# Optimization experiments

Hardware: AMD Instinct MI355X
Metric: run time of the kernel (lower is better)

The kernel has to match this reference:

```python
import jax, jax.numpy as jnp
import numpy as np

N = 500000   # active voxels
CIN = 32
COUT = 64
K = 27       # 3^3 kernel offsets
M = 250000   # kernel-map pairs per offset
EPS = 1e-5


def setup_inputs() -> dict:
    key = jax.random.key(0)
    ks = jax.random.split(key, 7)
    feats = jax.random.normal(ks[0], (N, CIN), dtype=jnp.float32)
    W = jax.random.normal(ks[1], (K, CIN, COUT), dtype=jnp.float32) / np.sqrt(K * CIN)
    gamma = jnp.ones((COUT,), dtype=jnp.float32)
    beta = jnp.zeros((COUT,), dtype=jnp.float32)
    run_mean = 0.1 * jax.random.normal(ks[2], (COUT,), dtype=jnp.float32)
    run_var = jax.random.uniform(ks[3], (COUT,), dtype=jnp.float32) + 0.5
    in_idx = jax.random.randint(ks[4], (K, M), 0, N, dtype=jnp.int32)
    out_idx = jax.random.randint(ks[5], (K, M), 0, N, dtype=jnp.int32)
    return {"feats": feats, "W": W, "gamma": gamma, "beta": beta,
            "run_mean": run_mean, "run_var": run_var,
            "in_idx": in_idx, "out_idx": out_idx}


def reference(feats, W, gamma, beta, run_mean, run_var, in_idx, out_idx):
    # Sparse 3D conv: for each kernel offset k, gather input rows, apply W[k],
    # scatter-accumulate into output rows (MinkowskiConvolution semantics).
    n_out = feats.shape[0]  # stride=1 -> same active sites

    def body(acc, xs):
        Wk, ik, ok = xs                      # [CIN,COUT], [M], [M]
        contrib = feats[ik] @ Wk             # gather + GEMM: [M, COUT]
        return acc.at[ok].add(contrib), None # scatter-accumulate

    out0 = jnp.zeros((n_out, COUT), dtype=feats.dtype)
    out, _ = jax.lax.scan(body, out0, (W, in_idx, out_idx))

    # BatchNorm (inference stats) + ReLU, fused elementwise epilogue
    inv = jax.lax.rsqrt(run_var + EPS)
    y = (out - run_mean) * (inv * gamma) + beta
    return jnp.maximum(y, 0.0)
```

## Files before the change

### kernel.cpp

```cpp
#include <hip/hip_runtime.h>

#define CIN  32
#define COUT 64
#define KOFF 27
#define EPS  1e-5f

__global__ __launch_bounds__(256) void conv_scatter(
    const float* __restrict__ feats,
    const float* __restrict__ W,
    const int*   __restrict__ in_idx,
    const int*   __restrict__ out_idx,
    float*       __restrict__ out,
    int M)
{
    __shared__ float Wl[CIN * COUT];
    const int k   = blockIdx.x;
    const int tid = threadIdx.x;

    const float* Wk = W + (size_t)k * (CIN * COUT);
    for (int i = tid; i < CIN * COUT; i += 256) Wl[i] = Wk[i];
    __syncthreads();

    const int lane = tid & 63;
    const int wave = tid >> 6;
    const int wavesTotal = gridDim.y * 4;
    const int* ikb = in_idx  + (size_t)k * M;
    const int* okb = out_idx + (size_t)k * M;

    for (int m = blockIdx.y * 4 + wave; m < M; m += wavesTotal) {
        const int ik = ikb[m];
        const int ok = okb[m];
        const float4* f4 = (const float4*)(feats + (size_t)ik * CIN);
        float acc = 0.f;
        #pragma unroll
        for (int c0 = 0; c0 < CIN / 4; ++c0) {
            float4 f = f4[c0];
            acc += f.x * Wl[(c0 * 4 + 0) * COUT + lane];
            acc += f.y * Wl[(c0 * 4 + 1) * COUT + lane];
            acc += f.z * Wl[(c0 * 4 + 2) * COUT + lane];
            acc += f.w * Wl[(c0 * 4 + 3) * COUT + lane];
        }
        atomicAdd(out + (size_t)ok * COUT + lane, acc);
    }
}

__global__ __launch_bounds__(256) void bn_relu(
    float* __restrict__ out,
    const float* __restrict__ gamma,
    const float* __restrict__ beta,
    const float* __restrict__ rmean,
    const float* __restrict__ rvar,
    int total4)
{
    __shared__ float scale[COUT], shift[COUT];
    if (threadIdx.x < COUT) {
        const int c = threadIdx.x;
        const float inv = rsqrtf(rvar[c] + EPS);
        const float s = inv * gamma[c];
        scale[c] = s;
        shift[c] = beta[c] - rmean[c] * s;
    }
    __syncthreads();

    const int stride = gridDim.x * blockDim.x;
    for (int i = blockIdx.x * blockDim.x + threadIdx.x; i < total4; i += stride) {
        float4 v = ((const float4*)out)[i];
        const int c0 = (i * 4) & (COUT - 1);
        v.x = fmaxf(v.x * scale[c0 + 0] + shift[c0 + 0], 0.f);
        v.y = fmaxf(v.y * scale[c0 + 1] + shift[c0 + 1], 0.f);
        v.z = fmaxf(v.z * scale[c0 + 2] + shift[c0 + 2], 0.f);
        v.w = fmaxf(v.w * scale[c0 + 3] + shift[c0 + 3], 0.f);
        ((float4*)out)[i] = v;
    }
}

extern "C" void kernel_launch(void* const* d_in, const int* in_sizes, int n_in,
                              void* d_out, int out_size, void* d_ws, size_t ws_size,
                              hipStream_t stream) {
    const float* feats  = (const float*)d_in[0];
    const float* W      = (const float*)d_in[1];
    const float* gamma  = (const float*)d_in[2];
    const float* beta   = (const float*)d_in[3];
    const float* rmean  = (const float*)d_in[4];
    const float* rvar   = (const float*)d_in[5];
    const int*   in_idx  = (const int*)d_in[6];
    const int*   out_idx = (const int*)d_in[7];
    float* out = (float*)d_out;

    const int N = in_sizes[0] / CIN;
    const int M = in_sizes[6] / KOFF;

    hipMemsetAsync(out, 0, (size_t)N * COUT * sizeof(float), stream);

    dim3 grid(KOFF, 512);
    conv_scatter<<<grid, 256, 0, stream>>>(feats, W, in_idx, out_idx, out, M);

    const int total4 = N * COUT / 4;
    int blocks = (total4 + 255) / 256;
    if (blocks > 2048) blocks = 2048;
    bn_relu<<<blocks, 256, 0, stream>>>(out, gamma, beta, rmean, rvar, total4);
}
```

Before: 2.236 ms.

## Bin kernel-map pairs by output tile and accumulate in shared memory

Adds a counting-sort pipeline (histogram, single-block scan, fill) that groups gather/scatter pairs by 256-row output tile and kernel offset, packing input index, offset and local row into one 32-bit record. A new conv kernel then accumulates each tile in LDS with shared atomics, holding that offset's weights in registers, and applies BN+ReLU before one coalesced write. This removes global float atomics, the output memset and the separate epilogue pass. In exchange it adds preprocessing kernels with global int atomics, a serial one-block scan, and a dependence on workspace size and N < 2^19 (otherwise it falls back to the old path).

```diff
diff --git a/kernel.cpp b/kernel.cpp
--- a/kernel.cpp
+++ b/kernel.cpp
@@ -3,73 +3,173 @@
 #define CIN  32
 #define COUT 64
 #define KOFF 27
+#define TILE 256
 #define EPS  1e-5f
 
+
+__global__ __launch_bounds__(256) void hist_kernel(
+    const int* __restrict__ out_idx, int* __restrict__ hist, int M)
+{
+    const int m = blockIdx.x * 256 + threadIdx.x;
+    const int k = blockIdx.y;
+    if (m < M) {
+        const int ok = out_idx[(size_t)k * M + m];
+        atomicAdd(&hist[(ok >> 8) * KOFF + k], 1);
+    }
+}
+
+__global__ __launch_bounds__(1024) void scan_kernel(
+    const int* __restrict__ hist, int* __restrict__ off, int* __restrict__ cur, int B)
+{
+    __shared__ int part[1024];
+    const int tid = threadIdx.x;
+    const int chunk = (B + 1023) / 1024;
+    const int base = tid * chunk;
+    int sum = 0;
+    for (int j = 0; j < chunk; ++j) { int i = base + j; if (i < B) sum += hist[i]; }
+    part[tid] = sum;
+    __syncthreads();
+    for (int d = 1; d < 1024; d <<= 1) {
+        int v = (tid >= d) ? part[tid - d] : 0;
+        __syncthreads();
+        part[tid] += v;
+        __syncthreads();
+    }
+    int run = part[tid] - sum;
+    for (int j = 0; j < chunk; ++j) {
+        int i = base + j;
+        if (i < B) { off[i] = run; cur[i] = run; run += hist[i]; }
+    }
+    if (tid == 1023) off[B] = run;
+}
+
+__global__ __launch_bounds__(256) void fill_kernel(
+    const int* __restrict__ in_idx, const int* __restrict__ out_idx,
+    int* __restrict__ cur, unsigned* __restrict__ recs, int M)
+{
+    const int m = blockIdx.x * 256 + threadIdx.x;
+    const int k = blockIdx.y;
+    if (m < M) {
+        const int ok  = out_idx[(size_t)k * M + m];
+        const int ik  = in_idx [(size_t)k * M + m];
+        const int bin = (ok >> 8) * KOFF + k;
+        const int pos = atomicAdd(&cur[bin], 1);
+        recs[pos] = (unsigned)ik | ((unsigned)k << 19) | ((unsigned)(ok & 255) << 24);
+    }
+}
+
+__global__ __launch_bounds__(512, 4) void conv_main(
+    const float* __restrict__ feats, const float* __restrict__ W,
+    const int* __restrict__ off, const unsigned* __restrict__ recs,
+    const float* __restrict__ gamma, const float* __restrict__ beta,
+    const float* __restrict__ rmean, const float* __restrict__ rvar,
+    float* __restrict__ out, int N)
+{
+    __shared__ float acc[TILE * COUT];
+    __shared__ float sc[COUT], sh[COUT];
+    const int tid  = threadIdx.x;
+    const int tile = blockIdx.x;
+
+    float4* acc4 = (float4*)acc;
+    for (int i = tid; i < TILE * COUT / 4; i += 512) acc4[i] = make_float4(0, 0, 0, 0);
+    if (tid < COUT) {
+        const float inv = rsqrtf(rvar[tid] + EPS);
+        const float s = inv * gamma[tid];
+        sc[tid] = s; sh[tid] = beta[tid] - rmean[tid] * s;
+    }
+    __syncthreads();
+
+    const int lane = tid & 63;
+    const int wave = tid >> 6;
+
+    for (int k = wave; k < KOFF; k += 8) {
+        const int seg = tile * KOFF + k;
+        const int s = off[seg], e = off[seg + 1];
+        if (s >= e) continue;
+        float w[CIN];
+        const float* Wk = W + (size_t)k * (CIN * COUT);
+        #pragma unroll
+        for (int c = 0; c < CIN; ++c) w[c] = Wk[c * COUT + lane];
+        for (int r = s; r < e; ++r) {
+            const unsigned rec = recs[r];
+            const int ik    = rec & 0x7FFFF;
+            const int local = rec >> 24;
+            const float4* f4 = (const float4*)(feats + (size_t)ik * CIN);
+            float a = 0.f;
+            #pragma unroll
+            for (int c4 = 0; c4 < CIN / 4; ++c4) {
+                const float4 f = f4[c4];
+                a += f.x * w[c4*4+0] + f.y * w[c4*4+1] + f.z * w[c4*4+2] + f.w * w[c4*4+3];
+            }
+            atomicAdd(&acc[local * COUT + lane], a);
+        }
+    }
+    __syncthreads();
+
+    const int base = tile * TILE;
+    for (int i = tid; i < TILE * COUT / 4; i += 512) {
+        const int row = i >> 4;
+        if (base + row < N) {
+            float4 v = acc4[i];
+            const int c0 = (i & 15) * 4;
+            v.x = fmaxf(v.x * sc[c0+0] + sh[c0+0], 0.f);
+            v.y = fmaxf(v.y * sc[c0+1] + sh[c0+1], 0.f);
+            v.z = fmaxf(v.z * sc[c0+2] + sh[c0+2], 0.f);
+            v.w = fmaxf(v.w * sc[c0+3] + sh[c0+3], 0.f);
+            ((float4*)out)[(size_t)base * (COUT / 4) + i] = v;
+        }
+    }
+}
+
+
 __global__ __launch_bounds__(256) void conv_scatter(
-    const float* __restrict__ feats,
-    const float* __restrict__ W,
-    const int*   __restrict__ in_idx,
-    const int*   __restrict__ out_idx,
-    float*       __restrict__ out,
-    int M)
+    const float* __restrict__ feats, const float* __restrict__ W,
+    const int* __restrict__ in_idx, const int* __restrict__ out_idx,
+    float* __restrict__ out, int M)
 {
     __shared__ float Wl[CIN * COUT];
-    const int k   = blockIdx.x;
-    const int tid = threadIdx.x;
-
+    const int k = blockIdx.x, tid = threadIdx.x;
     const float* Wk = W + (size_t)k * (CIN * COUT);
     for (int i = tid; i < CIN * COUT; i += 256) Wl[i] = Wk[i];
     __syncthreads();
-
-    const int lane = tid & 63;
-    const int wave = tid >> 6;
+    const int lane = tid & 63, wave = tid >> 6;
     const int wavesTotal = gridDim.y * 4;
-    const int* ikb = in_idx  + (size_t)k * M;
+    const int* ikb = in_idx + (size_t)k * M;
     const int* okb = out_idx + (size_t)k * M;
-
     for (int m = blockIdx.y * 4 + wave; m < M; m += wavesTotal) {
-        const int ik = ikb[m];
-        const int ok = okb[m];
+        const int ik = ikb[m], ok = okb[m];
         const float4* f4 = (const float4*)(feats + (size_t)ik * CIN);
         float acc = 0.f;
         #pragma unroll
         for (int c0 = 0; c0 < CIN / 4; ++c0) {
             float4 f = f4[c0];
-            acc += f.x * Wl[(c0 * 4 + 0) * COUT + lane];
-            acc += f.y * Wl[(c0 * 4 + 1) * COUT + lane];
-            acc += f.z * Wl[(c0 * 4 + 2) * COUT + lane];
-            acc += f.w * Wl[(c0 * 4 + 3) * COUT + lane];
+            acc += f.x * Wl[(c0*4+0)*COUT + lane] + f.y * Wl[(c0*4+1)*COUT + lane]
+                 + f.z * Wl[(c0*4+2)*COUT + lane] + f.w * Wl[(c0*4+3)*COUT + lane];
         }
         atomicAdd(out + (size_t)ok * COUT + lane, acc);
     }
 }
 
 __global__ __launch_bounds__(256) void bn_relu(
-    float* __restrict__ out,
-    const float* __restrict__ gamma,
-    const float* __restrict__ beta,
-    const float* __restrict__ rmean,
-    const float* __restrict__ rvar,
-    int total4)
+    float* __restrict__ out, const float* __restrict__ gamma, const float* __restrict__ beta,
+    const float* __restrict__ rmean, const float* __restrict__ rvar, int total4)
 {
     __shared__ float scale[COUT], shift[COUT];
     if (threadIdx.x < COUT) {
         const int c = threadIdx.x;
         const float inv = rsqrtf(rvar[c] + EPS);
         const float s = inv * gamma[c];
-        scale[c] = s;
-        shift[c] = beta[c] - rmean[c] * s;
-    }
-    __syncthreads();
-
+        scale[c] = s; shift[c] = beta[c] - rmean[c] * s;
+    }
+    __syncthreads();
     const int stride = gridDim.x * blockDim.x;
     for (int i = blockIdx.x * blockDim.x + threadIdx.x; i < total4; i += stride) {
         float4 v = ((const float4*)out)[i];
         const int c0 = (i * 4) & (COUT - 1);
-        v.x = fmaxf(v.x * scale[c0 + 0] + shift[c0 + 0], 0.f);
-        v.y = fmaxf(v.y * scale[c0 + 1] + shift[c0 + 1], 0.f);
-        v.z = fmaxf(v.z * scale[c0 + 2] + shift[c0 + 2], 0.f);
-        v.w = fmaxf(v.w * scale[c0 + 3] + shift[c0 + 3], 0.f);
+        v.x = fmaxf(v.x * scale[c0+0] + shift[c0+0], 0.f);
+        v.y = fmaxf(v.y * scale[c0+1] + shift[c0+1], 0.f);
+        v.z = fmaxf(v.z * scale[c0+2] + shift[c0+2], 0.f);
+        v.w = fmaxf(v.w * scale[c0+3] + shift[c0+3], 0.f);
         ((float4*)out)[i] = v;
     }
 }
@@ -89,14 +189,31 @@
 
     const int N = in_sizes[0] / CIN;
     const int M = in_sizes[6] / KOFF;
-
-    hipMemsetAsync(out, 0, (size_t)N * COUT * sizeof(float), stream);
-
-    dim3 grid(KOFF, 512);
-    conv_scatter<<<grid, 256, 0, stream>>>(feats, W, in_idx, out_idx, out, M);
-
-    const int total4 = N * COUT / 4;
-    int blocks = (total4 + 255) / 256;
-    if (blocks > 2048) blocks = 2048;
-    bn_relu<<<blocks, 256, 0, stream>>>(out, gamma, beta, rmean, rvar, total4);
-}
+    const int ntiles = (N + TILE - 1) / TILE;
+    const int B = ntiles * KOFF;
+    const size_t total_pairs = (size_t)KOFF * M;
+    const size_t needed = (size_t)(3 * B + 1) * 4 + total_pairs * 4;
+
+    if (ws_size >= needed && N < (1 << 19)) {
+        int* hist = (int*)d_ws;
+        int* off  = hist + B;
+        int* cur  = off + B + 1;
+        unsigned* recs = (unsigned*)(cur + B);
+
+        hipMemsetAsync(hist, 0, (size_t)B * 4, stream);
+        dim3 g((M + 255) / 256, KOFF);
+        hist_kernel<<<g, 256, 0, stream>>>(out_idx, hist, M);
+        scan_kernel<<<1, 1024, 0, stream>>>(hist, off, cur, B);
+        fill_kernel<<<g, 256, 0, stream>>>(in_idx, out_idx, cur, recs, M);
+        conv_main<<<ntiles, 512, 0, stream>>>(feats, W, off, recs,
+                                              gamma, beta, rmean, rvar, out, N);
+    } else {
+        hipMemsetAsync(out, 0, (size_t)N * COUT * sizeof(float), stream);
+        dim3 grid(KOFF, 512);
+        conv_scatter<<<grid, 256, 0, stream>>>(feats, W, in_idx, out_idx, out, M);
+        const int total4 = N * COUT / 4;
+        int blocks = (total4 + 255) / 256;
+        if (blocks > 2048) blocks = 2048;
+        bn_relu<<<blocks, 256, 0, stream>>>(out, gamma, beta, rmean, rvar, total4);
+    }
+}
```

Result: slower. 3.377 ms (+51.0%).
